# Kernel tuning notes

Hardware: AMD Instinct MI355X
Metric: run time of the kernel (lower is better)

## Reference

```python
import jax, jax.numpy as jnp
import numpy as np

B, N, MAX_DEG = 256, 512, 6
F_IN, H = 62, 128  # layers = [62, 128, 128]
NUM_DEG = MAX_DEG + 1  # degree buckets 0..6


def gather_neighbors(atoms, edges, maskvalue):
    # atoms [B,N,F], edges [B,N,D] with -1 padding -> [B,N,D,F]
    idx = jnp.maximum(edges, 0)
    neigh = jax.vmap(lambda a, e: a[e])(atoms, idx)
    return jnp.where(edges[..., None] < 0, jnp.asarray(maskvalue, atoms.dtype), neigh)


def nfp_conv(atoms, edges, W, b):
    # W [NUM_DEG, F_in, F_out], b [NUM_DEG, F_out]
    deg = jnp.sum(edges >= 0, axis=-1)  # [B,N]
    neigh = gather_neighbors(atoms, edges, 0.0)
    summed = neigh.sum(axis=2) + atoms  # include self, [B,N,F_in]
    out = jnp.zeros(summed.shape[:2] + (W.shape[-1],), summed.dtype)
    for d in range(NUM_DEG):  # small fixed set of degree buckets
        h = jax.nn.sigmoid(summed @ W[d] + b[d])
        out = out + h * (deg == d)[..., None].astype(h.dtype)
    return out


def graph_pool(atoms, edges):
    # max over self + neighbors
    neigh = gather_neighbors(atoms, edges, -jnp.inf)
    allf = jnp.concatenate([atoms[:, :, None, :], neigh], axis=2)  # [B,N,D+1,F]
    return allf.max(axis=2)


def setup_inputs() -> dict:
    key = jax.random.key(0)
    ka, ke, km, k0, k1, k2, k3 = jax.random.split(key, 7)
    a = jax.random.normal(ka, (B, N, F_IN), dtype=jnp.float32)
    e = jax.random.randint(ke, (B, N, MAX_DEG), 0, N, dtype=jnp.int32)
    # introduce -1 padding so atoms have varied degrees 0..6
    u = jax.random.uniform(km, (B, N, MAX_DEG))
    e = jnp.where(u < 0.6, e, -1).astype(jnp.int32)
    W0 = jax.random.normal(k0, (NUM_DEG, F_IN, H), dtype=jnp.float32) * 0.1
    b0 = jax.random.normal(k1, (NUM_DEG, H), dtype=jnp.float32) * 0.1
    W1 = jax.random.normal(k2, (NUM_DEG, H, H), dtype=jnp.float32) * 0.1
    b1 = jax.random.normal(k3, (NUM_DEG, H), dtype=jnp.float32) * 0.1
    return {"a": a, "e": e, "W0": W0, "b0": b0, "W1": W1, "b1": b1}


def reference(a, e, W0, b0, W1, b1):
    x = nfp_conv(a, e, W0, b0)
    x = graph_pool(x, e)
    x = nfp_conv(x, e, W1, b1)
    x = graph_pool(x, e)
    return x.sum(axis=1)  # SubgraphSum: [B, H]
```

## Files before the change

### kernel.cpp

```cpp
#include <hip/hip_runtime.h>
#include <math.h>

#define BB 256
#define NN 512
#define DD 6
#define F_IN 62
#define HH 128
#define ND 7
#define TOTAL (BB*NN)
#define OPB 640
#define GPB 40
#define TPB 10

typedef __bf16 bf16x8 __attribute__((ext_vector_type(8)));
typedef float f32x4 __attribute__((ext_vector_type(4)));

__device__ __forceinline__ unsigned short f2bf(float f) {
    unsigned u = __builtin_bit_cast(unsigned, f);
    u = (u + 0x7FFFu + ((u >> 16) & 1u)) >> 16;
    return (unsigned short)u;
}
__device__ __forceinline__ float lo2f(unsigned x) { return __builtin_bit_cast(float, x << 16); }
__device__ __forceinline__ float hi2f(unsigned x) { return __builtin_bit_cast(float, x & 0xFFFF0000u); }


__global__ __launch_bounds__(512) void k_sort16(const int* __restrict__ e,
                                                int* __restrict__ order,
                                                int* __restrict__ dgrp,
                                                int* __restrict__ ntiles) {
    __shared__ unsigned int scnt[ND];
    __shared__ unsigned int sbase[ND + 1];
    const int b = blockIdx.x;
    const int t = threadIdx.x;
    if (t < ND) scnt[t] = 0u;
    for (int i = t; i < OPB; i += 512) order[b * OPB + i] = -1;
    __syncthreads();
    int d = 0;
#pragma unroll
    for (int j = 0; j < DD; ++j) d += (e[(b * NN + t) * DD + j] >= 0) ? 1 : 0;
    unsigned rk = atomicAdd(&scnt[d], 1u);
    __syncthreads();
    if (t == 0) {
        unsigned acc = 0;
        for (int k = 0; k < ND; ++k) { sbase[k] = acc; acc += (scnt[k] + 15u) & ~15u; }
        sbase[ND] = acc;
        for (int k = 0; k < ND; ++k)
            for (unsigned g = sbase[k] >> 4; g < (sbase[k + 1] >> 4); ++g)
                dgrp[b * GPB + g] = k;
        for (unsigned g = acc >> 4; g < GPB; ++g) dgrp[b * GPB + g] = 0;
        ntiles[b] = (int)((acc + 63u) >> 6);
    }
    __syncthreads();
    order[b * OPB + sbase[d] + rk] = t;
}


__global__ __launch_bounds__(256) void k_prep_a(const float* __restrict__ a,
                                                unsigned short* __restrict__ Ap) {
    int u = blockIdx.x * 256 + threadIdx.x;
    int r = u >> 3;
    int c0 = (u & 7) * 8;
    unsigned short h[8];
#pragma unroll
    for (int i = 0; i < 8; ++i) {
        int c = c0 + i;
        h[i] = (c < F_IN) ? f2bf(a[(size_t)r * F_IN + c]) : (unsigned short)0;
    }
    uint4 p;
    p.x = (unsigned)h[0] | ((unsigned)h[1] << 16);
    p.y = (unsigned)h[2] | ((unsigned)h[3] << 16);
    p.z = (unsigned)h[4] | ((unsigned)h[5] << 16);
    p.w = (unsigned)h[6] | ((unsigned)h[7] << 16);
    *(uint4*)&Ap[(size_t)r * 64 + c0] = p;
}


__global__ void k_prep_wt(const float* __restrict__ W, unsigned short* __restrict__ WT,
                          int F, int K) {
    int n = blockIdx.x;
    int d = blockIdx.y;
    for (int k = threadIdx.x; k < K; k += 64) {
        float v = (k < F) ? W[((size_t)d * F + k) * HH + n] : 0.f;
        WT[((size_t)d * HH + n) * K + k] = f2bf(v);
    }
}


template<int KB, int THREADS>
__global__ __launch_bounds__(THREADS, 8)
void k_conv_mfma(const unsigned short* __restrict__ Xp,
                 const int* __restrict__ e,
                 const unsigned short* __restrict__ WT,
                 const float* __restrict__ bias,
                 const int* __restrict__ order,
                 const int* __restrict__ dgrp,
                 const int* __restrict__ ntiles,
                 unsigned short* __restrict__ Y) {
    constexpr int K = KB * 8;
    constexpr int LOGKB = (KB == 16) ? 4 : 3;
    constexpr int WAVES = THREADS / 64;
    constexpr int SUBW = WAVES / 4;
    constexpr int CPW = 128 / SUBW;
    constexpr int NFR = CPW / 16;
    __shared__ unsigned short sP[64 * 128];
    __shared__ int vT[64];
    __shared__ int eT[64 * DD];

    const int t = threadIdx.x;
    const int l = t & 63;
    const int w = t >> 6;

    const int bi = blockIdx.x;
    const int x8 = bi & 7;
    const int j = bi >> 3;
    const int batch = x8 + 8 * (j / TPB);
    const int tile = j % TPB;
    if (tile >= ntiles[batch]) return;

    if (t < 64) vT[t] = order[batch * OPB + tile * 64 + t];
    __syncthreads();
    if (t < 64 * DD) {
        int v = vT[t / DD];
        eT[t] = (v >= 0) ? e[((size_t)batch * NN + v) * DD + (t % DD)] : -1;
    }
    __syncthreads();

    {
        const int kb = t & (KB - 1);
        const int n = t >> LOGKB;
        const int v = vT[n];
        float s[8] = {0.f, 0.f, 0.f, 0.f, 0.f, 0.f, 0.f, 0.f};
        if (v >= 0) {
            const unsigned short* base = Xp + (size_t)batch * NN * K + kb * 8;
            uint4 p = *(const uint4*)(base + (size_t)v * K);
            s[0] = lo2f(p.x); s[1] = hi2f(p.x); s[2] = lo2f(p.y); s[3] = hi2f(p.y);
            s[4] = lo2f(p.z); s[5] = hi2f(p.z); s[6] = lo2f(p.w); s[7] = hi2f(p.w);
#pragma unroll
            for (int jj = 0; jj < DD; ++jj) {
                int idx = eT[n * DD + jj];
                if (idx >= 0) {
                    uint4 q = *(const uint4*)(base + (size_t)idx * K);
                    s[0] += lo2f(q.x); s[1] += hi2f(q.x); s[2] += lo2f(q.y); s[3] += hi2f(q.y);
                    s[4] += lo2f(q.z); s[5] += hi2f(q.z); s[6] += lo2f(q.w); s[7] += hi2f(q.w);
                }
            }
        }
        uint4 r;
        r.x = (unsigned)f2bf(s[0]) | ((unsigned)f2bf(s[1]) << 16);
        r.y = (unsigned)f2bf(s[2]) | ((unsigned)f2bf(s[3]) << 16);
        r.z = (unsigned)f2bf(s[4]) | ((unsigned)f2bf(s[5]) << 16);
        r.w = (unsigned)f2bf(s[6]) | ((unsigned)f2bf(s[7]) << 16);
        *(uint4*)&sP[(n * KB + (kb ^ (n & 7))) * 8] = r;
    }
    __syncthreads();

    const int lr = l & 15;
    const int lq = l >> 4;
    const int mb = w / SUBW;
    const int col0 = (w % SUBW) * CPW;
    const int d = dgrp[batch * GPB + tile * 4 + mb];
    const int nrow = mb * 16 + lr;

    bf16x8 af[K / 32];
#pragma unroll
    for (int kk = 0; kk < K / 32; ++kk)
        af[kk] = *(const bf16x8*)&sP[(nrow * KB + ((kk * 4 + lq) ^ (nrow & 7))) * 8];

    f32x4 acc[NFR];
#pragma unroll
    for (int fr = 0; fr < NFR; ++fr) { f32x4 z = {0.f, 0.f, 0.f, 0.f}; acc[fr] = z; }
#pragma unroll
    for (int fr = 0; fr < NFR; ++fr) {
        const unsigned short* wp = WT + ((size_t)d * HH + col0 + fr * 16 + lr) * K + lq * 8;
#pragma unroll
        for (int kk = 0; kk < K / 32; ++kk) {
            bf16x8 bfr = *(const bf16x8*)(wp + kk * 32);
            acc[fr] = __builtin_amdgcn_mfma_f32_16x16x32_bf16(af[kk], bfr, acc[fr], 0, 0, 0);
        }
    }

    __syncthreads();
#pragma unroll
    for (int fr = 0; fr < NFR; ++fr) {
        const int col = col0 + fr * 16 + lr;
        const float bv = bias[d * HH + col];
#pragma unroll
        for (int r = 0; r < 4; ++r) {
            const int n = mb * 16 + lq * 4 + r;
            float z = 1.f / (1.f + __expf(-(acc[fr][r] + bv)));
            sP[n * HH + col] = f2bf(z);
        }
    }
    __syncthreads();
    for (int u = t; u < 1024; u += THREADS) {
        int n = u >> 4;
        int c8 = (u & 15) * 8;
        int v = vT[n];
        if (v >= 0) {
            uint4 p = *(const uint4*)&sP[n * HH + c8];
            *(uint4*)&Y[((size_t)batch * NN + v) * HH + c8] = p;
        }
    }
}


__global__ __launch_bounds__(256) void k_pool_bf(const unsigned short* __restrict__ X,
                                                 const int* __restrict__ e,
                                                 unsigned short* __restrict__ P) {
    const int t = threadIdx.x;
    const int bi = blockIdx.x;
    const int x8 = bi & 7;
    const int j = bi >> 3;
    const int batch = x8 + 8 * (j >> 5);
    const int sub = j & 31;
    const int u = batch * NN + sub * 16 + (t >> 4);
    const int c8 = (t & 15) * 8;
    const int nbase = u & ~(NN - 1);
    float m[8];
    {
        uint4 p = *(const uint4*)(X + (size_t)u * HH + c8);
        m[0] = lo2f(p.x); m[1] = hi2f(p.x); m[2] = lo2f(p.y); m[3] = hi2f(p.y);
        m[4] = lo2f(p.z); m[5] = hi2f(p.z); m[6] = lo2f(p.w); m[7] = hi2f(p.w);
    }
#pragma unroll
    for (int jj = 0; jj < DD; ++jj) {
        int idx = e[u * DD + jj];
        if (idx >= 0) {
            uint4 p = *(const uint4*)(X + (size_t)(nbase + idx) * HH + c8);
            m[0] = fmaxf(m[0], lo2f(p.x)); m[1] = fmaxf(m[1], hi2f(p.x));
            m[2] = fmaxf(m[2], lo2f(p.y)); m[3] = fmaxf(m[3], hi2f(p.y));
            m[4] = fmaxf(m[4], lo2f(p.z)); m[5] = fmaxf(m[5], hi2f(p.z));
            m[6] = fmaxf(m[6], lo2f(p.w)); m[7] = fmaxf(m[7], hi2f(p.w));
        }
    }
    uint4 r;
    r.x = (unsigned)f2bf(m[0]) | ((unsigned)f2bf(m[1]) << 16);
    r.y = (unsigned)f2bf(m[2]) | ((unsigned)f2bf(m[3]) << 16);
    r.z = (unsigned)f2bf(m[4]) | ((unsigned)f2bf(m[5]) << 16);
    r.w = (unsigned)f2bf(m[6]) | ((unsigned)f2bf(m[7]) << 16);
    *(uint4*)&P[(size_t)u * HH + c8] = r;
}


__global__ __launch_bounds__(256) void k_pool_sum_part(const unsigned short* __restrict__ X,
                                                       const int* __restrict__ e,
                                                       float* __restrict__ partial) {
    __shared__ float red[16][HH + 4];
    const int t = threadIdx.x;
    const int bi = blockIdx.x;
    const int x8 = bi & 7;
    const int j = bi >> 3;
    const int b = x8 + 8 * (j >> 5);
    const int chunk = j & 31;
    const int slot = t >> 4;
    const int c8 = (t & 15) * 8;

    const int u = b * NN + chunk * 16 + slot;
    float m[8];
    {
        uint4 p = *(const uint4*)(X + (size_t)u * HH + c8);
        m[0] = lo2f(p.x); m[1] = hi2f(p.x); m[2] = lo2f(p.y); m[3] = hi2f(p.y);
        m[4] = lo2f(p.z); m[5] = hi2f(p.z); m[6] = lo2f(p.w); m[7] = hi2f(p.w);
    }
#pragma unroll
    for (int jj = 0; jj < DD; ++jj) {
        int idx = e[u * DD + jj];
        if (idx >= 0) {
            uint4 q = *(const uint4*)(X + (size_t)(b * NN + idx) * HH + c8);
            m[0] = fmaxf(m[0], lo2f(q.x)); m[1] = fmaxf(m[1], hi2f(q.x));
            m[2] = fmaxf(m[2], lo2f(q.y)); m[3] = fmaxf(m[3], hi2f(q.y));
            m[4] = fmaxf(m[4], lo2f(q.z)); m[5] = fmaxf(m[5], hi2f(q.z));
            m[6] = fmaxf(m[6], lo2f(q.w)); m[7] = fmaxf(m[7], hi2f(q.w));
        }
    }
#pragma unroll
    for (int i = 0; i < 8; ++i) red[slot][c8 + i] = m[i];
    __syncthreads();
    if (t < HH) {
        float s = 0.f;
#pragma unroll
        for (int k = 0; k < 16; ++k) s += red[k][t];
        partial[((size_t)b * 32 + chunk) * HH + t] = s;
    }
}


__global__ __launch_bounds__(256) void k_sum_final(const float* __restrict__ partial,
                                                   float* __restrict__ out) {
    int g = blockIdx.x * 256 + threadIdx.x;
    int b = g >> 7;
    int c = g & 127;
    float s = 0.f;
#pragma unroll
    for (int k = 0; k < 32; ++k) s += partial[((size_t)b * 32 + k) * HH + c];
    out[g] = s;
}


extern "C" void kernel_launch(void* const* d_in, const int* in_sizes, int n_in,
                              void* d_out, int out_size, void* d_ws, size_t ws_size,
                              hipStream_t stream) {
    const float* a  = (const float*)d_in[0];
    const int*   e  = (const int*)d_in[1];
    const float* W0 = (const float*)d_in[2];
    const float* b0 = (const float*)d_in[3];
    const float* W1 = (const float*)d_in[4];
    const float* b1 = (const float*)d_in[5];
    float* out = (float*)d_out;

    char* ws = (char*)d_ws;
    const size_t XB = (size_t)TOTAL * HH * 2;
    unsigned short* xbuf = (unsigned short*)ws;
    unsigned short* pbuf = (unsigned short*)(ws + XB);
    unsigned short* Ap   = (unsigned short*)(ws + 2 * XB);
    float* partial = (float*)Ap;
    unsigned short* WT0  = (unsigned short*)(ws + 2 * XB + (size_t)TOTAL * 64 * 2);
    unsigned short* WT1  = WT0 + (size_t)ND * HH * 64;
    char* ip = (char*)(WT1 + (size_t)ND * HH * 128);
    int* order  = (int*)ip;
    int* dgrp   = (int*)(ip + (size_t)BB * OPB * 4);
    int* ntiles = (int*)(ip + (size_t)BB * (OPB + GPB) * 4);

    hipLaunchKernelGGL(k_sort16, dim3(BB), dim3(NN), 0, stream, e, order, dgrp, ntiles);

    hipLaunchKernelGGL(k_prep_a, dim3(TOTAL * 8 / 256), dim3(256), 0, stream, a, Ap);
    hipLaunchKernelGGL(k_prep_wt, dim3(HH, ND), dim3(64), 0, stream, W0, WT0, F_IN, 64);
    hipLaunchKernelGGL(k_prep_wt, dim3(HH, ND), dim3(64), 0, stream, W1, WT1, HH, HH);

    hipLaunchKernelGGL((k_conv_mfma<8, 512>),   dim3(BB * TPB), dim3(512), 0, stream,
                       Ap, e, WT0, b0, order, dgrp, ntiles, xbuf);
    hipLaunchKernelGGL(k_pool_bf, dim3(TOTAL / 16), dim3(256), 0, stream, xbuf, e, pbuf);
    hipLaunchKernelGGL((k_conv_mfma<16, 1024>), dim3(BB * TPB), dim3(1024), 0, stream,
                       pbuf, e, WT1, b1, order, dgrp, ntiles, xbuf);
    hipLaunchKernelGGL(k_pool_sum_part, dim3(BB * 32), dim3(256), 0, stream, xbuf, e, partial);
    hipLaunchKernelGGL(k_sum_final, dim3(BB * HH / 256), dim3(256), 0, stream, partial, out);
}
```

Baseline: 169.8 us.

## Split neighbor gather out of conv GEMM into separate sorted-order gather kernels

Moves the neighbor-sum gather out of the MFMA conv kernels into standalone gather kernels. These write summed rows in degree-sorted slot order, so the GEMM kernel only streams contiguous rows into shared memory. Layer 1 now gathers directly from fp32 input, which removes the separate bf16 conversion pass. Layer 2's GEMM drops from 1024 to 512 threads. The split adds extra global round-trips for the gathered buffers and one more launch, in exchange for better occupancy and less latency-bound work inside the GEMM.

```diff
diff --git a/kernel.cpp b/kernel.cpp
--- a/kernel.cpp
+++ b/kernel.cpp
@@ -23,6 +23,25 @@
 __device__ __forceinline__ float lo2f(unsigned x) { return __builtin_bit_cast(float, x << 16); }
 __device__ __forceinline__ float hi2f(unsigned x) { return __builtin_bit_cast(float, x & 0xFFFF0000u); }
 
+__device__ __forceinline__ uint4 pack8(const float* s) {
+    uint4 r;
+    r.x = (unsigned)f2bf(s[0]) | ((unsigned)f2bf(s[1]) << 16);
+    r.y = (unsigned)f2bf(s[2]) | ((unsigned)f2bf(s[3]) << 16);
+    r.z = (unsigned)f2bf(s[4]) | ((unsigned)f2bf(s[5]) << 16);
+    r.w = (unsigned)f2bf(s[6]) | ((unsigned)f2bf(s[7]) << 16);
+    return r;
+}
+__device__ __forceinline__ void unpack_add(float* s, uint4 q) {
+    s[0] += lo2f(q.x); s[1] += hi2f(q.x); s[2] += lo2f(q.y); s[3] += hi2f(q.y);
+    s[4] += lo2f(q.z); s[5] += hi2f(q.z); s[6] += lo2f(q.w); s[7] += hi2f(q.w);
+}
+__device__ __forceinline__ void unpack_max(float* s, uint4 q) {
+    s[0] = fmaxf(s[0], lo2f(q.x)); s[1] = fmaxf(s[1], hi2f(q.x));
+    s[2] = fmaxf(s[2], lo2f(q.y)); s[3] = fmaxf(s[3], hi2f(q.y));
+    s[4] = fmaxf(s[4], lo2f(q.z)); s[5] = fmaxf(s[5], hi2f(q.z));
+    s[6] = fmaxf(s[6], lo2f(q.w)); s[7] = fmaxf(s[7], hi2f(q.w));
+}
+
 
 __global__ __launch_bounds__(512) void k_sort16(const int* __restrict__ e,
                                                 int* __restrict__ order,
@@ -55,26 +74,6 @@
 }
 
 
-__global__ __launch_bounds__(256) void k_prep_a(const float* __restrict__ a,
-                                                unsigned short* __restrict__ Ap) {
-    int u = blockIdx.x * 256 + threadIdx.x;
-    int r = u >> 3;
-    int c0 = (u & 7) * 8;
-    unsigned short h[8];
-#pragma unroll
-    for (int i = 0; i < 8; ++i) {
-        int c = c0 + i;
-        h[i] = (c < F_IN) ? f2bf(a[(size_t)r * F_IN + c]) : (unsigned short)0;
-    }
-    uint4 p;
-    p.x = (unsigned)h[0] | ((unsigned)h[1] << 16);
-    p.y = (unsigned)h[2] | ((unsigned)h[3] << 16);
-    p.z = (unsigned)h[4] | ((unsigned)h[5] << 16);
-    p.w = (unsigned)h[6] | ((unsigned)h[7] << 16);
-    *(uint4*)&Ap[(size_t)r * 64 + c0] = p;
-}
-
-
 __global__ void k_prep_wt(const float* __restrict__ W, unsigned short* __restrict__ WT,
                           int F, int K) {
     int n = blockIdx.x;
@@ -86,25 +85,87 @@
 }
 
 
-template<int KB, int THREADS>
-__global__ __launch_bounds__(THREADS, 8)
-void k_conv_mfma(const unsigned short* __restrict__ Xp,
-                 const int* __restrict__ e,
-                 const unsigned short* __restrict__ WT,
-                 const float* __restrict__ bias,
-                 const int* __restrict__ order,
-                 const int* __restrict__ dgrp,
-                 const int* __restrict__ ntiles,
-                 unsigned short* __restrict__ Y) {
+__global__ __launch_bounds__(512)
+void k_gather1(const float* __restrict__ a, const int* __restrict__ e,
+               const int* __restrict__ order, const int* __restrict__ ntiles,
+               unsigned short* __restrict__ S1) {
+    const int t = threadIdx.x;
+    const int bi = blockIdx.x;
+    const int x8 = bi & 7;
+    const int j = bi >> 3;
+    const int batch = x8 + 8 * (j / TPB);
+    const int blk = j % TPB;
+    if (blk >= ntiles[batch]) return;
+    const int slot = blk * 64 + (t >> 3);
+    const int kb = t & 7;
+    const int v = order[batch * OPB + slot];
+    if (v < 0) return;
+    const int* ep = e + ((size_t)batch * NN + v) * DD;
+    const float* base = a + (size_t)batch * NN * F_IN;
+    float s[8] = {0.f, 0.f, 0.f, 0.f, 0.f, 0.f, 0.f, 0.f};
+    {
+        const float* r = base + (size_t)v * F_IN + kb * 8;
+        float2 z0 = *(const float2*)(r);     s[0] += z0.x; s[1] += z0.y;
+        float2 z1 = *(const float2*)(r + 2); s[2] += z1.x; s[3] += z1.y;
+        float2 z2 = *(const float2*)(r + 4); s[4] += z2.x; s[5] += z2.y;
+        if (kb < 7) { float2 z3 = *(const float2*)(r + 6); s[6] += z3.x; s[7] += z3.y; }
+    }
+#pragma unroll
+    for (int jj = 0; jj < DD; ++jj) {
+        int idx = ep[jj];
+        if (idx >= 0) {
+            const float* r = base + (size_t)idx * F_IN + kb * 8;
+            float2 z0 = *(const float2*)(r);     s[0] += z0.x; s[1] += z0.y;
+            float2 z1 = *(const float2*)(r + 2); s[2] += z1.x; s[3] += z1.y;
+            float2 z2 = *(const float2*)(r + 4); s[4] += z2.x; s[5] += z2.y;
+            if (kb < 7) { float2 z3 = *(const float2*)(r + 6); s[6] += z3.x; s[7] += z3.y; }
+        }
+    }
+    *(uint4*)(S1 + ((size_t)batch * OPB + slot) * 64 + kb * 8) = pack8(s);
+}
+
+
+__global__ __launch_bounds__(512)
+void k_gather2(const unsigned short* __restrict__ P1, const int* __restrict__ e,
+               const int* __restrict__ order, const int* __restrict__ ntiles,
+               unsigned short* __restrict__ S2m, unsigned short* __restrict__ S2p) {
+    constexpr int BPB2 = 20;
+    const int t = threadIdx.x;
+    const int bi = blockIdx.x;
+    const int x8 = bi & 7;
+    const int j = bi >> 3;
+    const int batch = x8 + 8 * (j / BPB2);
+    const int blk = j % BPB2;
+    if ((blk >> 1) >= ntiles[batch]) return;
+    const int slot = blk * 32 + (t >> 4);
+    const int kb = t & 15;
+    const int v = order[batch * OPB + slot];
+    if (v < 0) return;
+    const int* ep = e + ((size_t)batch * NN + v) * DD;
+    const unsigned short* base = P1 + (size_t)batch * NN * HH + kb * 8;
+    float s[8] = {0.f, 0.f, 0.f, 0.f, 0.f, 0.f, 0.f, 0.f};
+    unpack_add(s, *(const uint4*)(base + (size_t)v * HH));
+#pragma unroll
+    for (int jj = 0; jj < DD; ++jj) {
+        int idx = ep[jj];
+        if (idx >= 0) unpack_add(s, *(const uint4*)(base + (size_t)idx * HH));
+    }
+    uint4 r = pack8(s);
+    if (slot < 512) *(uint4*)(S2m + ((size_t)batch * 512 + slot) * HH + kb * 8) = r;
+    else            *(uint4*)(S2p + ((size_t)batch * 128 + (slot - 512)) * HH + kb * 8) = r;
+}
+
+
+template<int KB>
+__global__ __launch_bounds__(512, 4)
+void k_gemm(const unsigned short* __restrict__ Sm, const unsigned short* __restrict__ Sp,
+            const unsigned short* __restrict__ WT, const float* __restrict__ bias,
+            const int* __restrict__ order, const int* __restrict__ dgrp,
+            const int* __restrict__ ntiles, unsigned short* __restrict__ Y) {
     constexpr int K = KB * 8;
     constexpr int LOGKB = (KB == 16) ? 4 : 3;
-    constexpr int WAVES = THREADS / 64;
-    constexpr int SUBW = WAVES / 4;
-    constexpr int CPW = 128 / SUBW;
-    constexpr int NFR = CPW / 16;
     __shared__ unsigned short sP[64 * 128];
     __shared__ int vT[64];
-    __shared__ int eT[64 * DD];
 
     const int t = threadIdx.x;
     const int l = t & 63;
@@ -118,46 +179,26 @@
     if (tile >= ntiles[batch]) return;
 
     if (t < 64) vT[t] = order[batch * OPB + tile * 64 + t];
-    __syncthreads();
-    if (t < 64 * DD) {
-        int v = vT[t / DD];
-        eT[t] = (v >= 0) ? e[((size_t)batch * NN + v) * DD + (t % DD)] : -1;
-    }
-    __syncthreads();
-
-    {
-        const int kb = t & (KB - 1);
-        const int n = t >> LOGKB;
-        const int v = vT[n];
-        float s[8] = {0.f, 0.f, 0.f, 0.f, 0.f, 0.f, 0.f, 0.f};
-        if (v >= 0) {
-            const unsigned short* base = Xp + (size_t)batch * NN * K + kb * 8;
-            uint4 p = *(const uint4*)(base + (size_t)v * K);
-            s[0] = lo2f(p.x); s[1] = hi2f(p.x); s[2] = lo2f(p.y); s[3] = hi2f(p.y);
-            s[4] = lo2f(p.z); s[5] = hi2f(p.z); s[6] = lo2f(p.w); s[7] = hi2f(p.w);
-#pragma unroll
-            for (int jj = 0; jj < DD; ++jj) {
-                int idx = eT[n * DD + jj];
-                if (idx >= 0) {
-                    uint4 q = *(const uint4*)(base + (size_t)idx * K);
-                    s[0] += lo2f(q.x); s[1] += hi2f(q.x); s[2] += lo2f(q.y); s[3] += hi2f(q.y);
-                    s[4] += lo2f(q.z); s[5] += hi2f(q.z); s[6] += lo2f(q.w); s[7] += hi2f(q.w);
-                }
-            }
-        }
-        uint4 r;
-        r.x = (unsigned)f2bf(s[0]) | ((unsigned)f2bf(s[1]) << 16);
-        r.y = (unsigned)f2bf(s[2]) | ((unsigned)f2bf(s[3]) << 16);
-        r.z = (unsigned)f2bf(s[4]) | ((unsigned)f2bf(s[5]) << 16);
-        r.w = (unsigned)f2bf(s[6]) | ((unsigned)f2bf(s[7]) << 16);
-        *(uint4*)&sP[(n * KB + (kb ^ (n & 7))) * 8] = r;
+
+    for (int u = t; u < 64 * KB; u += 512) {
+        const int n = u >> LOGKB;
+        const int kb = u & (KB - 1);
+        const int slot = tile * 64 + n;
+        const unsigned short* src;
+        if constexpr (KB == 16) {
+            src = (slot < 512) ? Sm + ((size_t)batch * 512 + slot) * K + kb * 8
+                               : Sp + ((size_t)batch * 128 + (slot - 512)) * K + kb * 8;
+        } else {
+            src = Sm + ((size_t)batch * OPB + slot) * K + kb * 8;
+        }
+        *(uint4*)&sP[(n * KB + (kb ^ (n & 7))) * 8] = *(const uint4*)src;
     }
     __syncthreads();
 
     const int lr = l & 15;
     const int lq = l >> 4;
-    const int mb = w / SUBW;
-    const int col0 = (w % SUBW) * CPW;
+    const int mb = w >> 1;
+    const int col0 = (w & 1) * 64;
     const int d = dgrp[batch * GPB + tile * 4 + mb];
     const int nrow = mb * 16 + lr;
 
@@ -166,11 +207,11 @@
     for (int kk = 0; kk < K / 32; ++kk)
         af[kk] = *(const bf16x8*)&sP[(nrow * KB + ((kk * 4 + lq) ^ (nrow & 7))) * 8];
 
-    f32x4 acc[NFR];
-#pragma unroll
-    for (int fr = 0; fr < NFR; ++fr) { f32x4 z = {0.f, 0.f, 0.f, 0.f}; acc[fr] = z; }
-#pragma unroll
-    for (int fr = 0; fr < NFR; ++fr) {
+    f32x4 acc[4];
+#pragma unroll
+    for (int fr = 0; fr < 4; ++fr) { f32x4 z = {0.f, 0.f, 0.f, 0.f}; acc[fr] = z; }
+#pragma unroll
+    for (int fr = 0; fr < 4; ++fr) {
         const unsigned short* wp = WT + ((size_t)d * HH + col0 + fr * 16 + lr) * K + lq * 8;
 #pragma unroll
         for (int kk = 0; kk < K / 32; ++kk) {
@@ -181,7 +222,7 @@
 
     __syncthreads();
 #pragma unroll
-    for (int fr = 0; fr < NFR; ++fr) {
+    for (int fr = 0; fr < 4; ++fr) {
         const int col = col0 + fr * 16 + lr;
         const float bv = bias[d * HH + col];
 #pragma unroll
@@ -192,7 +233,7 @@
         }
     }
     __syncthreads();
-    for (int u = t; u < 1024; u += THREADS) {
+    for (int u = t; u < 1024; u += 512) {
         int n = u >> 4;
         int c8 = (u & 15) * 8;
         int v = vT[n];
@@ -225,20 +266,9 @@
 #pragma unroll
     for (int jj = 0; jj < DD; ++jj) {
         int idx = e[u * DD + jj];
-        if (idx >= 0) {
-            uint4 p = *(const uint4*)(X + (size_t)(nbase + idx) * HH + c8);
-            m[0] = fmaxf(m[0], lo2f(p.x)); m[1] = fmaxf(m[1], hi2f(p.x));
-            m[2] = fmaxf(m[2], lo2f(p.y)); m[3] = fmaxf(m[3], hi2f(p.y));
-            m[4] = fmaxf(m[4], lo2f(p.z)); m[5] = fmaxf(m[5], hi2f(p.z));
-            m[6] = fmaxf(m[6], lo2f(p.w)); m[7] = fmaxf(m[7], hi2f(p.w));
-        }
-    }
-    uint4 r;
-    r.x = (unsigned)f2bf(m[0]) | ((unsigned)f2bf(m[1]) << 16);
-    r.y = (unsigned)f2bf(m[2]) | ((unsigned)f2bf(m[3]) << 16);
-    r.z = (unsigned)f2bf(m[4]) | ((unsigned)f2bf(m[5]) << 16);
-    r.w = (unsigned)f2bf(m[6]) | ((unsigned)f2bf(m[7]) << 16);
-    *(uint4*)&P[(size_t)u * HH + c8] = r;
+        if (idx >= 0) unpack_max(m, *(const uint4*)(X + (size_t)(nbase + idx) * HH + c8));
+    }
+    *(uint4*)&P[(size_t)u * HH + c8] = pack8(m);
 }
 
 
@@ -265,13 +295,7 @@
 #pragma unroll
     for (int jj = 0; jj < DD; ++jj) {
         int idx = e[u * DD + jj];
-        if (idx >= 0) {
-            uint4 q = *(const uint4*)(X + (size_t)(b * NN + idx) * HH + c8);
-            m[0] = fmaxf(m[0], lo2f(q.x)); m[1] = fmaxf(m[1], hi2f(q.x));
-            m[2] = fmaxf(m[2], lo2f(q.y)); m[3] = fmaxf(m[3], hi2f(q.y));
-            m[4] = fmaxf(m[4], lo2f(q.z)); m[5] = fmaxf(m[5], hi2f(q.z));
-            m[6] = fmaxf(m[6], lo2f(q.w)); m[7] = fmaxf(m[7], hi2f(q.w));
-        }
+        if (idx >= 0) unpack_max(m, *(const uint4*)(X + (size_t)(b * NN + idx) * HH + c8));
     }
 #pragma unroll
     for (int i = 0; i < 8; ++i) red[slot][c8 + i] = m[i];
@@ -309,29 +333,31 @@
     float* out = (float*)d_out;
 
     char* ws = (char*)d_ws;
-    const size_t XB = (size_t)TOTAL * HH * 2;
-    unsigned short* xbuf = (unsigned short*)ws;
-    unsigned short* pbuf = (unsigned short*)(ws + XB);
-    unsigned short* Ap   = (unsigned short*)(ws + 2 * XB);
-    float* partial = (float*)Ap;
-    unsigned short* WT0  = (unsigned short*)(ws + 2 * XB + (size_t)TOTAL * 64 * 2);
-    unsigned short* WT1  = WT0 + (size_t)ND * HH * 64;
-    char* ip = (char*)(WT1 + (size_t)ND * HH * 128);
-    int* order  = (int*)ip;
-    int* dgrp   = (int*)(ip + (size_t)BB * OPB * 4);
-    int* ntiles = (int*)(ip + (size_t)BB * (OPB + GPB) * 4);
+    const size_t MB32 = (size_t)TOTAL * HH * 2;
+    unsigned short* bufA = (unsigned short*)ws;
+    unsigned short* bufB = (unsigned short*)(ws + MB32);
+    unsigned short* S2p  = (unsigned short*)(ws + 2 * MB32);
+    float* partial = (float*)S2p;
+    char* dp = ws + 2 * MB32 + (size_t)BB * 128 * HH * 2;
+    unsigned short* WT0 = (unsigned short*)dp;
+    unsigned short* WT1 = WT0 + (size_t)ND * HH * 64;
+    int* order  = (int*)(WT1 + (size_t)ND * HH * 128);
+    int* dgrp   = order + (size_t)BB * OPB;
+    int* ntiles = dgrp + (size_t)BB * GPB;
 
     hipLaunchKernelGGL(k_sort16, dim3(BB), dim3(NN), 0, stream, e, order, dgrp, ntiles);
-
-    hipLaunchKernelGGL(k_prep_a, dim3(TOTAL * 8 / 256), dim3(256), 0, stream, a, Ap);
     hipLaunchKernelGGL(k_prep_wt, dim3(HH, ND), dim3(64), 0, stream, W0, WT0, F_IN, 64);
     hipLaunchKernelGGL(k_prep_wt, dim3(HH, ND), dim3(64), 0, stream, W1, WT1, HH, HH);
 
-    hipLaunchKernelGGL((k_conv_mfma<8, 512>),   dim3(BB * TPB), dim3(512), 0, stream,
-                       Ap, e, WT0, b0, order, dgrp, ntiles, xbuf);
-    hipLaunchKernelGGL(k_pool_bf, dim3(TOTAL / 16), dim3(256), 0, stream, xbuf, e, pbuf);
-    hipLaunchKernelGGL((k_conv_mfma<16, 1024>), dim3(BB * TPB), dim3(1024), 0, stream,
-                       pbuf, e, WT1, b1, order, dgrp, ntiles, xbuf);
-    hipLaunchKernelGGL(k_pool_sum_part, dim3(BB * 32), dim3(256), 0, stream, xbuf, e, partial);
+    hipLaunchKernelGGL(k_gather1, dim3(BB * TPB), dim3(512), 0, stream,
+                       a, e, order, ntiles, bufB);
+    hipLaunchKernelGGL((k_gemm<8>), dim3(BB * TPB), dim3(512), 0, stream,
+                       bufB, (const unsigned short*)nullptr, WT0, b0, order, dgrp, ntiles, bufA);
+    hipLaunchKernelGGL(k_pool_bf, dim3(TOTAL / 16), dim3(256), 0, stream, bufA, e, bufB);
+    hipLaunchKernelGGL(k_gather2, dim3(BB * 20), dim3(512), 0, stream,
+                       bufB, e, order, ntiles, bufA, S2p);
+    hipLaunchKernelGGL((k_gemm<16>), dim3(BB * TPB), dim3(512), 0, stream,
+                       bufA, S2p, WT1, b1, order, dgrp, ntiles, bufB);
+    hipLaunchKernelGGL(k_pool_sum_part, dim3(BB * 32), dim3(256), 0, stream, bufB, e, partial);
     hipLaunchKernelGGL(k_sum_final, dim3(BB * HH / 256), dim3(256), 0, stream, partial, out);
 }
```

New measurement: 172.5 us. No clear change (+1.6%).
